# Kernel optimization log

Measured on AMD Instinct MI355X. Metric: run time of the kernel, lower is better.

The kernel has to match this reference:

```python
import jax, jax.numpy as jnp
import numpy as np

# DeepSpeed FixedSparsityConfig defaults (attention='unidirectional')
BLOCK = 16
NUM_LOCAL_BLOCKS = 4   # local window = 4 blocks = 64 tokens
D_MODEL = 1024
N_HEADS = 16
HEAD_DIM = D_MODEL // N_HEADS


def _block_layout(seq_len: int) -> np.ndarray:
    """Token-level boolean mask [S,S] from the fixed unidirectional block layout.
    Allowed iff: (same 4-block local window AND block_k <= block_q) OR
                 (block_k % 4 == 3 AND block_k <= block_q)  (causal global column).
    Same layout for every head (different_layout_per_head=False)."""
    nb = seq_len // BLOCK
    r = np.arange(nb)
    causal = r[None, :] <= r[:, None]
    same_win = (r[:, None] // NUM_LOCAL_BLOCKS) == (r[None, :] // NUM_LOCAL_BLOCKS)
    glob = (r[None, :] % NUM_LOCAL_BLOCKS) == (NUM_LOCAL_BLOCKS - 1)
    layout = (same_win & causal) | (glob & causal)
    return np.kron(layout, np.ones((BLOCK, BLOCK), dtype=bool))


def setup_inputs() -> dict:
    key = jax.random.key(0)
    ks = jax.random.split(key, 7)
    B, S = 2, 2048
    init = 1.0 / np.sqrt(D_MODEL)
    x = jax.random.normal(ks[0], (B, S, D_MODEL), jnp.float32)
    key_padding_mask = jnp.zeros((B, S), jnp.float32)  # additive mask ('add' mode)
    Wq = jax.random.normal(ks[1], (D_MODEL, D_MODEL), jnp.float32) * init
    Wk = jax.random.normal(ks[2], (D_MODEL, D_MODEL), jnp.float32) * init
    Wv = jax.random.normal(ks[3], (D_MODEL, D_MODEL), jnp.float32) * init
    bq = jax.random.normal(ks[4], (D_MODEL,), jnp.float32) * 0.01
    bk = jax.random.normal(ks[5], (D_MODEL,), jnp.float32) * 0.01
    bv = jax.random.normal(ks[6], (D_MODEL,), jnp.float32) * 0.01
    return dict(x=x, key_padding_mask=key_padding_mask,
                Wq=Wq, bq=bq, Wk=Wk, bk=bk, Wv=Wv, bv=bv)


def reference(x, key_padding_mask, Wq, bq, Wk, bk, Wv, bv):
    B, S, D = x.shape
    q = (x @ Wq + bq).reshape(B, S, N_HEADS, HEAD_DIM)
    k = (x @ Wk + bk).reshape(B, S, N_HEADS, HEAD_DIM)
    v = (x @ Wv + bv).reshape(B, S, N_HEADS, HEAD_DIM)
    scale = HEAD_DIM ** -0.5  # DeepSpeed scales by head_size**-0.5 inside softmax
    scores = jnp.einsum('bqhd,bkhd->bhqk', q, k) * scale
    scores = scores + key_padding_mask[:, None, None, :]
    mask = jnp.asarray(_block_layout(S))  # [S,S] bool; absent blocks excluded from softmax
    scores = jnp.where(mask[None, None], scores, -jnp.inf)
    attn = jax.nn.softmax(scores, axis=-1)
    out = jnp.einsum('bhqk,bkhd->bqhd', attn, v)
    return out.reshape(B, S, D)
```

## Files before the change

### kernel.cpp

```cpp
#include <hip/hip_runtime.h>
#include <hip/hip_bf16.h>

typedef __bf16 bf16;
typedef __bf16 bf16x4 __attribute__((ext_vector_type(4)));
typedef __bf16 bf16x8 __attribute__((ext_vector_type(8)));
typedef float  f32x4  __attribute__((ext_vector_type(4)));

#define D_MODEL 1024
#define S_LEN   2048
#define BATCH   2
#define NH      16
#define HD      64
#define NX ((size_t)BATCH * S_LEN * D_MODEL)

__device__ inline void gl_lds16(const bf16* g, bf16* l) {
    __builtin_amdgcn_global_load_lds(
        (const __attribute__((address_space(1))) void*)g,
        (__attribute__((address_space(3))) void*)l, 16, 0, 0);
}

__global__ __launch_bounds__(256) void prep(
    const float* __restrict__ x, bf16* __restrict__ xb,
    const float* __restrict__ Wq, const float* __restrict__ Wk,
    const float* __restrict__ Wv, bf16* __restrict__ Wt)
{
    __shared__ bf16 tile[64 * 72];

    if (blockIdx.x < 2048) {
        const size_t base = ((size_t)blockIdx.x * 256 + threadIdx.x) * 8;
        const float4 a = *(const float4*)(x + base);
        const float4 b = *(const float4*)(x + base + 4);
        bf16x8 o;
        o[0] = (bf16)a.x; o[1] = (bf16)a.y; o[2] = (bf16)a.z; o[3] = (bf16)a.w;
        o[4] = (bf16)b.x; o[5] = (bf16)b.y; o[6] = (bf16)b.z; o[7] = (bf16)b.w;
        *(bf16x8*)(xb + base) = o;
        return;
    }

    const int id2 = blockIdx.x - 2048;
    const int z = id2 >> 8;
    const float* W = (z == 0) ? Wq : (z == 1) ? Wk : Wv;
    const int k0 = ((id2 >> 4) & 15) * 64, n0 = (id2 & 15) * 64;

    const int r16 = threadIdx.x >> 4, c4 = (threadIdx.x & 15) << 2;

#pragma unroll
    for (int rr = 0; rr < 4; ++rr) {
        const int row = rr * 16 + r16;
        const float4 v = *(const float4*)(W + (size_t)(k0 + row) * D_MODEL + n0 + c4);
        bf16x4 o; o[0] = (bf16)v.x; o[1] = (bf16)v.y; o[2] = (bf16)v.z; o[3] = (bf16)v.w;
        *(bf16x4*)(tile + row * 72 + c4) = o;
    }
    __syncthreads();
#pragma unroll
    for (int rr = 0; rr < 4; ++rr) {
        const int row = rr * 16 + r16;
        bf16x4 o;
#pragma unroll
        for (int j = 0; j < 4; ++j) o[j] = tile[(c4 + j) * 72 + row];
        *(bf16x4*)(Wt + (size_t)(z * D_MODEL + n0 + row) * D_MODEL + k0 + c4) = o;
    }
}

#define GNT 32

__device__ __forceinline__ void stage_A(
    const bf16* __restrict__ Xb, bf16* __restrict__ sA,
    int m0, int k0, int tid, int wave)
{
    const int ci0 = tid;
    const int r0 = ci0 >> 2, c0 = (ci0 & 3) ^ ((ci0 >> 3) & 3);
    gl_lds16(Xb + (size_t)(m0 + r0) * D_MODEL + k0 + c0 * 8, sA + wave * 512);
    const int ci1 = 256 + tid;
    const int r1 = ci1 >> 2, c1 = (ci1 & 3) ^ ((ci1 >> 3) & 3);
    gl_lds16(Xb + (size_t)(m0 + r1) * D_MODEL + k0 + c1 * 8, sA + 2048 + wave * 512);
}

__device__ __forceinline__ void stage_B(
    const bf16* __restrict__ Wt, bf16* __restrict__ sB,
    int n0, int k0, int tid, int wave)
{
#pragma unroll
    for (int p = 0; p < 3; ++p) {
        const int ci = p * 256 + tid;
        const int r = ci >> 2, c = (ci & 3) ^ ((ci >> 3) & 3);
        gl_lds16(Wt + (size_t)(n0 + r) * D_MODEL + k0 + c * 8, sB + p * 2048 + wave * 512);
    }
}

template<int VM>
__device__ __forceinline__ void gemm_tile_body(
    const bf16* __restrict__ Xb, const bf16* __restrict__ Wt,
    bf16* __restrict__ As, bf16* __restrict__ Bs,
    int m0, int n0, int t, int tid, int wave, int wm, int wn,
    int col, int pchunk, f32x4 (&acc)[4][6])
{
    if constexpr (VM == 10)     asm volatile("s_waitcnt vmcnt(10)" ::: "memory");
    else if constexpr (VM == 5) asm volatile("s_waitcnt vmcnt(5)" ::: "memory");
    else                        asm volatile("s_waitcnt vmcnt(0)" ::: "memory");
    asm volatile("s_barrier" ::: "memory");

    const bf16* bufA = As + (t & 3) * 4096;
    const bf16* bufB = Bs + (t & 3) * 6144;
    const bool pf = (t + 3 < GNT);
    const int k3 = (t + 3) * 32;

    if (pf) stage_A(Xb, As + ((t + 3) & 3) * 4096, m0, k3, tid, wave);

    bf16x8 a[4], b[6];
#pragma unroll
    for (int mr = 0; mr < 4; ++mr)
        a[mr] = *(const bf16x8*)(bufA + (wm * 64 + mr * 16 + col) * 32 + pchunk * 8);
#pragma unroll
    for (int nr = 0; nr < 3; ++nr)
        b[nr] = *(const bf16x8*)(bufB + (wn * 96 + nr * 16 + col) * 32 + pchunk * 8);

    __builtin_amdgcn_s_setprio(1);
#pragma unroll
    for (int mr = 0; mr < 4; ++mr)
#pragma unroll
        for (int nr = 0; nr < 3; ++nr)
            acc[mr][nr] = __builtin_amdgcn_mfma_f32_16x16x32_bf16(a[mr], b[nr], acc[mr][nr], 0, 0, 0);
    __builtin_amdgcn_s_setprio(0);

    asm volatile("s_barrier" ::: "memory");
    if (pf) stage_B(Wt, Bs + ((t + 3) & 3) * 6144, n0, k3, tid, wave);
#pragma unroll
    for (int nr = 3; nr < 6; ++nr)
        b[nr] = *(const bf16x8*)(bufB + (wn * 96 + nr * 16 + col) * 32 + pchunk * 8);

    __builtin_amdgcn_s_setprio(1);
#pragma unroll
    for (int mr = 0; mr < 4; ++mr)
#pragma unroll
        for (int nr = 3; nr < 6; ++nr)
            acc[mr][nr] = __builtin_amdgcn_mfma_f32_16x16x32_bf16(a[mr], b[nr], acc[mr][nr], 0, 0, 0);
    __builtin_amdgcn_s_setprio(0);
}

__global__ __launch_bounds__(256, 2) void gemm_qkv_dp(
    const bf16* __restrict__ Xb, const bf16* __restrict__ Wt,
    const float* __restrict__ bq, const float* __restrict__ bk,
    const float* __restrict__ bv, bf16* __restrict__ QKV)
{
    extern __shared__ bf16 smem[];
    bf16* As = smem;
    bf16* Bs = smem + 16384;

    const int bid = blockIdx.x, k = bid & 7, j = bid >> 3;
    const int my = ((k & 3) << 3) + (j & 7);
    const int nx = ((k >> 2) << 3) + (j >> 3);
    const int m0 = my * 128, n0 = nx * 192;

    const int tid = threadIdx.x, wave = tid >> 6, lane = tid & 63;
    const int wm = wave >> 1, wn = wave & 1;
    const int col = lane & 15, quad = lane >> 4;
    const int pchunk = quad ^ ((col >> 1) & 3);

    f32x4 acc[4][6] = {};

    stage_A(Xb, As,         m0,  0, tid, wave);  stage_B(Wt, Bs,         n0,  0, tid, wave);
    stage_A(Xb, As + 4096,  m0, 32, tid, wave);  stage_B(Wt, Bs + 6144,  n0, 32, tid, wave);
    stage_A(Xb, As + 8192,  m0, 64, tid, wave);  stage_B(Wt, Bs + 12288, n0, 64, tid, wave);

    for (int t = 0; t < GNT - 2; ++t)
        gemm_tile_body<10>(Xb, Wt, As, Bs, m0, n0, t, tid, wave, wm, wn, col, pchunk, acc);
    gemm_tile_body<5>(Xb, Wt, As, Bs, m0, n0, GNT - 2, tid, wave, wm, wn, col, pchunk, acc);
    gemm_tile_body<0>(Xb, Wt, As, Bs, m0, n0, GNT - 1, tid, wave, wm, wn, col, pchunk, acc);

#pragma unroll
    for (int nr = 0; nr < 6; ++nr) {
        const int cg = n0 + wn * 96 + nr * 16 + col;
        const int z = cg >> 10, c = cg & 1023;
        const float bsv = (z == 0 ? bq : (z == 1 ? bk : bv))[c];
        const float scale = (z == 0) ? 0.125f : 1.0f;
        bf16* C = QKV + (size_t)z * NX;
#pragma unroll
        for (int mr = 0; mr < 4; ++mr)
#pragma unroll
            for (int i = 0; i < 4; ++i) {
                const int rg = m0 + wm * 64 + mr * 16 + quad * 4 + i;
                C[(size_t)rg * D_MODEL + c] = (bf16)((acc[mr][nr][i] + bsv) * scale);
            }
    }
}

__global__ __launch_bounds__(256, 4) void sparse_attn64(
    const bf16* __restrict__ Q, const bf16* __restrict__ Kv,
    const bf16* __restrict__ Vv, const float* __restrict__ kpm,
    float* __restrict__ out)
{
    const int lid = blockIdx.x + 32 * (blockIdx.y + 16 * blockIdx.z);
    const int xk = lid & 7, j = lid >> 3;
    const int pair = xk * 4 + (j & 3);
    const int h = pair & 15, b = pair >> 4;
    const int w = 31 - (j >> 2);

    const int t = threadIdx.x, wavei = t >> 6, lane = t & 63;
    const int col = lane & 15, quad = lane >> 4;
    const int qb = 4 * w + wavei;

    __shared__ bf16 KbS[64 * 72];
    __shared__ bf16 VtS[2][64 * 72];
    __shared__ bf16 Ps[4][16 * 72];

    const size_t qrow = ((size_t)(b * S_LEN + qb * 16 + col)) * D_MODEL + h * HD;
    const bf16x8 aq0 = *(const bf16x8*)(Q + qrow + quad * 8);
    const bf16x8 aq1 = *(const bf16x8*)(Q + qrow + 32 + quad * 8);

    f32x4 o[4] = {};
    float lacc[4] = {0.f, 0.f, 0.f, 0.f};

    const int nGlob = (w + 3) >> 2;
    const int niter = nGlob + 1;

    const int srow = t >> 2, sd16 = (t & 3) << 4;
    const int sg = srow >> 4, sr = srow & 15;
    const int p2 = t & 31, dg8 = (t >> 5) << 3;
    const int key0 = 2 * p2, vg = key0 >> 4, vr = key0 & 15;

    auto kb_of = [&](int it, int g) -> int {
        if (it >= nGlob) return 4 * w + g;
        const int jj = 4 * it + g;
        return (jj < w) ? (4 * jj + 3) : 3;
    };

    bf16x8 rk0, rk1, rv0, rv1;
    {
        const size_t krow = ((size_t)(b * S_LEN + kb_of(0, sg) * 16 + sr)) * D_MODEL + h * HD + sd16;
        rk0 = *(const bf16x8*)(Kv + krow);
        rk1 = *(const bf16x8*)(Kv + krow + 8);
        const size_t vrow = ((size_t)(b * S_LEN + kb_of(0, vg) * 16 + vr)) * D_MODEL + h * HD + dg8;
        rv0 = *(const bf16x8*)(Vv + vrow);
        rv1 = *(const bf16x8*)(Vv + vrow + D_MODEL);
        *(bf16x8*)(KbS + srow * 72 + sd16)     = rk0;
        *(bf16x8*)(KbS + srow * 72 + sd16 + 8) = rk1;
#pragma unroll
        for (int jj = 0; jj < 8; ++jj) {
            bf16 pr[2] = { rv0[jj], rv1[jj] };
            *(unsigned int*)(VtS[0] + (dg8 + jj) * 72 + key0) = *(unsigned int*)pr;
        }
    }

    for (int it = 0; it < niter; ++it) {
        __syncthreads();
        const int cur = it & 1, nxt = cur ^ 1;
        const bool more = (it + 1 < niter);
        if (more) {
            const size_t krow = ((size_t)(b * S_LEN + kb_of(it + 1, sg) * 16 + sr)) * D_MODEL + h * HD + sd16;
            rk0 = *(const bf16x8*)(Kv + krow);
            rk1 = *(const bf16x8*)(Kv + krow + 8);
            const size_t vrow = ((size_t)(b * S_LEN + kb_of(it + 1, vg) * 16 + vr)) * D_MODEL + h * HD + dg8;
            rv0 = *(const bf16x8*)(Vv + vrow);
            rv1 = *(const bf16x8*)(Vv + vrow + D_MODEL);
        }

        f32x4 s[4];
        float mval[4];
        bool  val[4];
#pragma unroll
        for (int g = 0; g < 4; ++g) {
            val[g] = (it == nGlob) ? (g <= wavei) : (4 * it + g < w);
            if (val[g]) {
                const int kb = kb_of(it, g);
                mval[g] = kpm[b * S_LEN + kb * 16 + col];
                f32x4 z = {};
                const bf16x8 bk0 = *(const bf16x8*)(KbS + (g * 16 + col) * 72 + quad * 8);
                const bf16x8 bk1 = *(const bf16x8*)(KbS + (g * 16 + col) * 72 + 32 + quad * 8);
                __builtin_amdgcn_s_setprio(1);
                z = __builtin_amdgcn_mfma_f32_16x16x32_bf16(aq0, bk0, z, 0, 0, 0);
                s[g] = __builtin_amdgcn_mfma_f32_16x16x32_bf16(aq1, bk1, z, 0, 0, 0);
                __builtin_amdgcn_s_setprio(0);
            }
        }

        __syncthreads();
        if (more) {
            *(bf16x8*)(KbS + srow * 72 + sd16)     = rk0;
            *(bf16x8*)(KbS + srow * 72 + sd16 + 8) = rk1;
        }

#pragma unroll
        for (int g = 0; g < 4; ++g) {
            if (val[g]) {
#pragma unroll
                for (int i = 0; i < 4; ++i) {
                    const float pv = __expf(s[g][i] + mval[g]);
                    lacc[i] += pv;
                    Ps[wavei][(quad * 4 + i) * 72 + g * 16 + col] = (bf16)pv;
                }
            } else {
#pragma unroll
                for (int i = 0; i < 4; ++i)
                    Ps[wavei][(quad * 4 + i) * 72 + g * 16 + col] = (bf16)0.0f;
            }
        }

        const bf16* Vt = VtS[cur];
        const bf16x8 aP0 = *(const bf16x8*)(Ps[wavei] + col * 72 + quad * 8);
        const bf16x8 aP1 = *(const bf16x8*)(Ps[wavei] + col * 72 + 32 + quad * 8);
        __builtin_amdgcn_s_setprio(1);
#pragma unroll
        for (int nt = 0; nt < 4; ++nt) {
            const bf16x8 b0 = *(const bf16x8*)(Vt + (nt * 16 + col) * 72 + quad * 8);
            const bf16x8 b1 = *(const bf16x8*)(Vt + (nt * 16 + col) * 72 + 32 + quad * 8);
            o[nt] = __builtin_amdgcn_mfma_f32_16x16x32_bf16(aP0, b0, o[nt], 0, 0, 0);
            o[nt] = __builtin_amdgcn_mfma_f32_16x16x32_bf16(aP1, b1, o[nt], 0, 0, 0);
        }
        __builtin_amdgcn_s_setprio(0);

        if (more) {
#pragma unroll
            for (int jj = 0; jj < 8; ++jj) {
                bf16 pr[2] = { rv0[jj], rv1[jj] };
                *(unsigned int*)(VtS[nxt] + (dg8 + jj) * 72 + key0) = *(unsigned int*)pr;
            }
        }
    }

#pragma unroll
    for (int i = 0; i < 4; ++i) {
        float rs = lacc[i];
        rs += __shfl_xor(rs, 1);
        rs += __shfl_xor(rs, 2);
        rs += __shfl_xor(rs, 4);
        rs += __shfl_xor(rs, 8);
        const float inv = 1.0f / rs;
        const int rg = b * S_LEN + qb * 16 + quad * 4 + i;
#pragma unroll
        for (int nt = 0; nt < 4; ++nt)
            out[(size_t)rg * D_MODEL + h * HD + nt * 16 + col] = o[nt][i] * inv;
    }
}

extern "C" void kernel_launch(void* const* d_in, const int* in_sizes, int n_in,
                              void* d_out, int out_size, void* d_ws, size_t ws_size,
                              hipStream_t stream)
{
    const float* x = nullptr; const float* kpm = nullptr;
    const float* Wp[3] = {nullptr, nullptr, nullptr};
    const float* bp[3] = {nullptr, nullptr, nullptr};
    int wn = 0, bn = 0;
    for (int i = 0; i < n_in; ++i) {
        const float* p = (const float*)d_in[i];
        const long s = in_sizes[i];
        if (s == (long)NX)            x = p;
        else if (s == BATCH * S_LEN)  kpm = p;
        else if (s == D_MODEL * D_MODEL && wn < 3) Wp[wn++] = p;
        else if (s == D_MODEL && bn < 3)           bp[bn++] = p;
    }

    bf16* Qb = (bf16*)d_ws;
    bf16* Kb = Qb + NX;
    bf16* Vb = Kb + NX;
    bf16* Xb = (bf16*)d_out;
    bf16* Wt = Xb + NX;
    float* outp = (float*)d_out;

    static bool attr_done = false;
    if (!attr_done) {
        (void)hipFuncSetAttribute(reinterpret_cast<const void*>(gemm_qkv_dp),
                                  hipFuncAttributeMaxDynamicSharedMemorySize, 81920);
        attr_done = true;
    }

    prep<<<2816, 256, 0, stream>>>(x, Xb, Wp[0], Wp[1], Wp[2], Wt);

    gemm_qkv_dp<<<dim3(512), 256, 81920, stream>>>(
        Xb, Wt, bp[0], bp[1], bp[2], Qb);

    sparse_attn64<<<dim3(S_LEN / 64, NH, BATCH), 256, 0, stream>>>(
        Qb, Kb, Vb, kpm, outp);
}
```

Baseline: 137.0 us.

## Shrink QKV GEMM tile to 128x128 with triple buffering and higher occupancy

The QKV projection GEMM moves from 128x192 tiles with a 4-stage LDS ring to 128x128 tiles with a 3-stage ring. LDS per block drops from 80KB to 48KB, so launch bounds go up to 3 blocks per CU and the grid grows from 512 to 768 blocks. The split mid-iteration barrier and the s_setprio hints are removed, and the epilogue now resolves bias and scale once per block because a 128-wide tile never crosses a Q/K/V boundary. The aim is better CU fill and latency hiding. The cost is less operand reuse per tile and a shallower prefetch pipeline.

```diff
diff --git a/kernel.cpp b/kernel.cpp
--- a/kernel.cpp
+++ b/kernel.cpp
@@ -64,28 +64,16 @@
 
 #define GNT 32
 
-__device__ __forceinline__ void stage_A(
-    const bf16* __restrict__ Xb, bf16* __restrict__ sA,
-    int m0, int k0, int tid, int wave)
+__device__ __forceinline__ void stage_128(
+    const bf16* __restrict__ src, bf16* __restrict__ dst,
+    int row0, int k0, int tid, int wave)
 {
     const int ci0 = tid;
     const int r0 = ci0 >> 2, c0 = (ci0 & 3) ^ ((ci0 >> 3) & 3);
-    gl_lds16(Xb + (size_t)(m0 + r0) * D_MODEL + k0 + c0 * 8, sA + wave * 512);
+    gl_lds16(src + (size_t)(row0 + r0) * D_MODEL + k0 + c0 * 8, dst + wave * 512);
     const int ci1 = 256 + tid;
     const int r1 = ci1 >> 2, c1 = (ci1 & 3) ^ ((ci1 >> 3) & 3);
-    gl_lds16(Xb + (size_t)(m0 + r1) * D_MODEL + k0 + c1 * 8, sA + 2048 + wave * 512);
-}
-
-__device__ __forceinline__ void stage_B(
-    const bf16* __restrict__ Wt, bf16* __restrict__ sB,
-    int n0, int k0, int tid, int wave)
-{
-#pragma unroll
-    for (int p = 0; p < 3; ++p) {
-        const int ci = p * 256 + tid;
-        const int r = ci >> 2, c = (ci & 3) ^ ((ci >> 3) & 3);
-        gl_lds16(Wt + (size_t)(n0 + r) * D_MODEL + k0 + c * 8, sB + p * 2048 + wave * 512);
-    }
+    gl_lds16(src + (size_t)(row0 + r1) * D_MODEL + k0 + c1 * 8, dst + 2048 + wave * 512);
 }
 
 template<int VM>
@@ -93,88 +81,76 @@
     const bf16* __restrict__ Xb, const bf16* __restrict__ Wt,
     bf16* __restrict__ As, bf16* __restrict__ Bs,
     int m0, int n0, int t, int tid, int wave, int wm, int wn,
-    int col, int pchunk, f32x4 (&acc)[4][6])
-{
-    if constexpr (VM == 10)     asm volatile("s_waitcnt vmcnt(10)" ::: "memory");
-    else if constexpr (VM == 5) asm volatile("s_waitcnt vmcnt(5)" ::: "memory");
-    else                        asm volatile("s_waitcnt vmcnt(0)" ::: "memory");
+    int col, int pchunk, f32x4 (&acc)[4][4])
+{
+    if constexpr (VM == 4) asm volatile("s_waitcnt vmcnt(4)" ::: "memory");
+    else                   asm volatile("s_waitcnt vmcnt(0)" ::: "memory");
     asm volatile("s_barrier" ::: "memory");
 
-    const bf16* bufA = As + (t & 3) * 4096;
-    const bf16* bufB = Bs + (t & 3) * 6144;
-    const bool pf = (t + 3 < GNT);
-    const int k3 = (t + 3) * 32;
-
-    if (pf) stage_A(Xb, As + ((t + 3) & 3) * 4096, m0, k3, tid, wave);
-
-    bf16x8 a[4], b[6];
+    const int cur = t % 3;
+    const bf16* bufA = As + cur * 4096;
+    const bf16* bufB = Bs + cur * 4096;
+
+    if (t + 2 < GNT) {
+        const int nslot = (t + 2) % 3;
+        const int k2 = (t + 2) * 32;
+        stage_128(Xb, As + nslot * 4096, m0, k2, tid, wave);
+        stage_128(Wt, Bs + nslot * 4096, n0, k2, tid, wave);
+    }
+
+    bf16x8 a[4], b[4];
 #pragma unroll
     for (int mr = 0; mr < 4; ++mr)
         a[mr] = *(const bf16x8*)(bufA + (wm * 64 + mr * 16 + col) * 32 + pchunk * 8);
 #pragma unroll
-    for (int nr = 0; nr < 3; ++nr)
-        b[nr] = *(const bf16x8*)(bufB + (wn * 96 + nr * 16 + col) * 32 + pchunk * 8);
-
-    __builtin_amdgcn_s_setprio(1);
+    for (int nr = 0; nr < 4; ++nr)
+        b[nr] = *(const bf16x8*)(bufB + (wn * 64 + nr * 16 + col) * 32 + pchunk * 8);
+
 #pragma unroll
     for (int mr = 0; mr < 4; ++mr)
 #pragma unroll
-        for (int nr = 0; nr < 3; ++nr)
+        for (int nr = 0; nr < 4; ++nr)
             acc[mr][nr] = __builtin_amdgcn_mfma_f32_16x16x32_bf16(a[mr], b[nr], acc[mr][nr], 0, 0, 0);
-    __builtin_amdgcn_s_setprio(0);
-
-    asm volatile("s_barrier" ::: "memory");
-    if (pf) stage_B(Wt, Bs + ((t + 3) & 3) * 6144, n0, k3, tid, wave);
-#pragma unroll
-    for (int nr = 3; nr < 6; ++nr)
-        b[nr] = *(const bf16x8*)(bufB + (wn * 96 + nr * 16 + col) * 32 + pchunk * 8);
-
-    __builtin_amdgcn_s_setprio(1);
-#pragma unroll
-    for (int mr = 0; mr < 4; ++mr)
-#pragma unroll
-        for (int nr = 3; nr < 6; ++nr)
-            acc[mr][nr] = __builtin_amdgcn_mfma_f32_16x16x32_bf16(a[mr], b[nr], acc[mr][nr], 0, 0, 0);
-    __builtin_amdgcn_s_setprio(0);
-}
-
-__global__ __launch_bounds__(256, 2) void gemm_qkv_dp(
+}
+
+__global__ __launch_bounds__(256, 3) void gemm_qkv_dp(
     const bf16* __restrict__ Xb, const bf16* __restrict__ Wt,
     const float* __restrict__ bq, const float* __restrict__ bk,
     const float* __restrict__ bv, bf16* __restrict__ QKV)
 {
     extern __shared__ bf16 smem[];
     bf16* As = smem;
-    bf16* Bs = smem + 16384;
+    bf16* Bs = smem + 12288;
 
     const int bid = blockIdx.x, k = bid & 7, j = bid >> 3;
     const int my = ((k & 3) << 3) + (j & 7);
-    const int nx = ((k >> 2) << 3) + (j >> 3);
-    const int m0 = my * 128, n0 = nx * 192;
+    const int nx = ((k >> 2) * 12) + (j >> 3);
+    const int m0 = my * 128, n0 = nx * 128;
 
     const int tid = threadIdx.x, wave = tid >> 6, lane = tid & 63;
     const int wm = wave >> 1, wn = wave & 1;
     const int col = lane & 15, quad = lane >> 4;
     const int pchunk = quad ^ ((col >> 1) & 3);
 
-    f32x4 acc[4][6] = {};
-
-    stage_A(Xb, As,         m0,  0, tid, wave);  stage_B(Wt, Bs,         n0,  0, tid, wave);
-    stage_A(Xb, As + 4096,  m0, 32, tid, wave);  stage_B(Wt, Bs + 6144,  n0, 32, tid, wave);
-    stage_A(Xb, As + 8192,  m0, 64, tid, wave);  stage_B(Wt, Bs + 12288, n0, 64, tid, wave);
-
-    for (int t = 0; t < GNT - 2; ++t)
-        gemm_tile_body<10>(Xb, Wt, As, Bs, m0, n0, t, tid, wave, wm, wn, col, pchunk, acc);
-    gemm_tile_body<5>(Xb, Wt, As, Bs, m0, n0, GNT - 2, tid, wave, wm, wn, col, pchunk, acc);
+    f32x4 acc[4][4] = {};
+
+    stage_128(Xb, As,        m0,  0, tid, wave);
+    stage_128(Wt, Bs,        n0,  0, tid, wave);
+    stage_128(Xb, As + 4096, m0, 32, tid, wave);
+    stage_128(Wt, Bs + 4096, n0, 32, tid, wave);
+
+    for (int t = 0; t < GNT - 1; ++t)
+        gemm_tile_body<4>(Xb, Wt, As, Bs, m0, n0, t, tid, wave, wm, wn, col, pchunk, acc);
     gemm_tile_body<0>(Xb, Wt, As, Bs, m0, n0, GNT - 1, tid, wave, wm, wn, col, pchunk, acc);
 
-#pragma unroll
-    for (int nr = 0; nr < 6; ++nr) {
-        const int cg = n0 + wn * 96 + nr * 16 + col;
-        const int z = cg >> 10, c = cg & 1023;
-        const float bsv = (z == 0 ? bq : (z == 1 ? bk : bv))[c];
-        const float scale = (z == 0) ? 0.125f : 1.0f;
-        bf16* C = QKV + (size_t)z * NX;
+    const int z = n0 >> 10, nc0 = n0 & 1023;
+    const float* bias = (z == 0) ? bq : (z == 1) ? bk : bv;
+    const float scale = (z == 0) ? 0.125f : 1.0f;
+    bf16* C = QKV + (size_t)z * NX;
+#pragma unroll
+    for (int nr = 0; nr < 4; ++nr) {
+        const int c = nc0 + wn * 64 + nr * 16 + col;
+        const float bsv = bias[c];
 #pragma unroll
         for (int mr = 0; mr < 4; ++mr)
 #pragma unroll
@@ -360,13 +336,13 @@
     static bool attr_done = false;
     if (!attr_done) {
         (void)hipFuncSetAttribute(reinterpret_cast<const void*>(gemm_qkv_dp),
-                                  hipFuncAttributeMaxDynamicSharedMemorySize, 81920);
+                                  hipFuncAttributeMaxDynamicSharedMemorySize, 49152);
         attr_done = true;
     }
 
     prep<<<2816, 256, 0, stream>>>(x, Xb, Wp[0], Wp[1], Wp[2], Wt);
 
-    gemm_qkv_dp<<<dim3(512), 256, 81920, stream>>>(
+    gemm_qkv_dp<<<dim3(768), 256, 49152, stream>>>(
         Xb, Wt, bp[0], bp[1], bp[2], Qb);
 
     sparse_attn64<<<dim3(S_LEN / 64, NH, BATCH), 256, 0, stream>>>(
```

Result: slower. 140.2 us (+2.3%).
